# Kernel tuning notes

Hardware: AMD Instinct MI355X
Metric: run time of the kernel (lower is better)

## Reference

```python
import jax, jax.numpy as jnp
import numpy as np

CHAN = 24
INNER = 64
GROUPS = 8
M = 5
LAM = 1e-4
MAX_ITER = 25
BETA = 1.0
EPS = 1e-5
B, HH, WW = 128, 32, 32


def conv2d(x, w, b=None):
    # NCHW, OIHW, 3x3 SAME conv (padding = kernel//2)
    y = jax.lax.conv_general_dilated(x, w, (1, 1), 'SAME',
                                     dimension_numbers=('NCHW', 'OIHW', 'NCHW'))
    if b is not None:
        y = y + b[None, :, None, None]
    return y


def group_norm(x, g, b):
    bsz, c, h, w = x.shape
    xg = x.reshape(bsz, GROUPS, c // GROUPS, h, w)
    mu = xg.mean(axis=(2, 3, 4), keepdims=True)
    var = xg.var(axis=(2, 3, 4), keepdims=True)
    xn = ((xg - mu) / jnp.sqrt(var + EPS)).reshape(bsz, c, h, w)
    return xn * g[None, :, None, None] + b[None, :, None, None]


def batch_norm(x, g, b):
    # training-mode batch statistics over (N, H, W)
    mu = x.mean(axis=(0, 2, 3), keepdims=True)
    var = x.var(axis=(0, 2, 3), keepdims=True)
    return (x - mu) / jnp.sqrt(var + EPS) * g[None, :, None, None] + b[None, :, None, None]


def resnet_f(p, z, x):
    c1w, g1g, g1b, c2w, g2g, g2b, g3g, g3b = p
    y = group_norm(jax.nn.relu(conv2d(z, c1w)), g1g, g1b)
    return group_norm(jax.nn.relu(z + group_norm(x + conv2d(y, c2w), g2g, g2b)), g3g, g3b)


def anderson(f, x0):
    # Anderson acceleration, fixed MAX_ITER iterations (no host-sync tol break).
    bsz = x0.shape[0]
    d = x0.size // bsz
    X = jnp.zeros((bsz, M, d), x0.dtype)
    Fm = jnp.zeros((bsz, M, d), x0.dtype)
    f0 = f(x0).reshape(bsz, -1)
    X = X.at[:, 0].set(x0.reshape(bsz, -1))
    Fm = Fm.at[:, 0].set(f0)
    X = X.at[:, 1].set(f0)
    Fm = Fm.at[:, 1].set(f(f0.reshape(x0.shape)).reshape(bsz, -1))
    for k in range(2, MAX_ITER):
        n = min(k, M)
        G = Fm[:, :n] - X[:, :n]                       # [b, n, d]
        Hm = jnp.zeros((bsz, n + 1, n + 1), x0.dtype)
        Hm = Hm.at[:, 0, 1:].set(1.0).at[:, 1:, 0].set(1.0)
        Hm = Hm.at[:, 1:, 1:].set(jnp.einsum('bnd,bmd->bnm', G, G)
                                  + LAM * jnp.eye(n, dtype=x0.dtype)[None])
        yv = jnp.zeros((bsz, n + 1, 1), x0.dtype).at[:, 0, 0].set(1.0)
        alpha = jnp.linalg.solve(Hm, yv)[:, 1:, 0]     # [b, n]
        xnew = (BETA * jnp.einsum('bn,bnd->bd', alpha, Fm[:, :n])
                + (1.0 - BETA) * jnp.einsum('bn,bnd->bd', alpha, X[:, :n]))
        X = X.at[:, k % M].set(xnew)
        Fm = Fm.at[:, k % M].set(f(xnew.reshape(x0.shape)).reshape(bsz, -1))
    return X[:, (MAX_ITER - 1) % M].reshape(x0.shape)


def setup_inputs() -> dict:
    key = jax.random.key(0)
    ks = jax.random.split(key, 8)
    inp = {
        'x': jax.random.normal(ks[0], (B, 3, HH, WW), jnp.float32),
        'pre_conv_w': jax.random.normal(ks[1], (CHAN, 3, 3, 3), jnp.float32) * 0.1,
        'pre_conv_b': jnp.zeros((CHAN,), jnp.float32),
        'pre_bn_g': jnp.ones((CHAN,), jnp.float32),
        'pre_bn_b': jnp.zeros((CHAN,), jnp.float32),
        'f_conv1_w': jax.random.normal(ks[2], (INNER, CHAN, 3, 3), jnp.float32) * 0.01,
        'gn1_g': jnp.ones((INNER,), jnp.float32),
        'gn1_b': jnp.zeros((INNER,), jnp.float32),
        'f_conv2_w': jax.random.normal(ks[3], (CHAN, INNER, 3, 3), jnp.float32) * 0.01,
        'gn2_g': jnp.ones((CHAN,), jnp.float32),
        'gn2_b': jnp.zeros((CHAN,), jnp.float32),
        'gn3_g': jnp.ones((CHAN,), jnp.float32),
        'gn3_b': jnp.zeros((CHAN,), jnp.float32),
        'post_bn_g': jnp.ones((CHAN,), jnp.float32),
        'post_bn_b': jnp.zeros((CHAN,), jnp.float32),
        'fc_w': jax.random.normal(ks[4], (10, CHAN * 4 * 4), jnp.float32) * 0.05,
        'fc_b': jnp.zeros((10,), jnp.float32),
    }
    return inp


def reference(x, pre_conv_w, pre_conv_b, pre_bn_g, pre_bn_b,
              f_conv1_w, gn1_g, gn1_b, f_conv2_w, gn2_g, gn2_b, gn3_g, gn3_b,
              post_bn_g, post_bn_b, fc_w, fc_b):
    # pre: conv + BatchNorm
    xp = batch_norm(conv2d(x, pre_conv_w, pre_conv_b), pre_bn_g, pre_bn_b)
    p = (f_conv1_w, gn1_g, gn1_b, f_conv2_w, gn2_g, gn2_b, gn3_g, gn3_b)
    # DEQ fixed-point solve (eval path: train=False returns the fixed point)
    z_star = anderson(lambda z: resnet_f(p, z, xp), jnp.zeros_like(xp))
    z = resnet_f(p, z_star, xp)
    # post: relu -> BN -> avgpool(8,8) -> flatten -> linear
    h = batch_norm(jax.nn.relu(z), post_bn_g, post_bn_b)
    bsz, c, hh, ww = h.shape
    pooled = h.reshape(bsz, c, hh // 8, 8, ww // 8, 8).mean(axis=(3, 5))  # [B,C,4,4]
    return pooled.reshape(bsz, -1) @ fc_w.T + fc_b
```

## Files before the change

### kernel.cpp

```cpp
#include <hip/hip_runtime.h>
#include <hip/hip_bf16.h>

typedef __hip_bfloat16 bf16;
typedef unsigned short ushortT;
typedef __attribute__((ext_vector_type(8))) short short8;
typedef __attribute__((ext_vector_type(4))) float f32x4;

#define BB 128
#define CHAN 24
#define INNER 64
#define HW 1024
#define DD (CHAN*HW)

constexpr size_t cBD = (size_t)BB*DD;
constexpr size_t cYB = (size_t)BB*INNER*HW;

__device__ __attribute__((aligned(16))) ushortT g_xp[cBD];
__device__ __attribute__((aligned(16))) ushortT g_X[5*cBD];
__device__ __attribute__((aligned(16))) ushortT g_F[5*cBD];
__device__ __attribute__((aligned(16))) ushortT g_G[5*cBD];
__device__ __attribute__((aligned(16))) ushortT g_yb[cYB];
__device__ __attribute__((aligned(16))) ushortT g_tb[cBD];
__device__ __attribute__((aligned(16))) ushortT g_w1m[9*64*32];
__device__ __attribute__((aligned(16))) ushortT g_w2m[9*24*64];
__device__ __attribute__((aligned(16))) float g_stats2a[48];
__device__ __attribute__((aligned(16))) float g_stats2b[48];
__device__ __attribute__((aligned(16))) float g_gn1sum[BB*8*2];
__device__ __attribute__((aligned(16))) float g_gn2sum[BB*24*2];
__device__ __attribute__((aligned(16))) float g_gram[BB*25];
__device__ __attribute__((aligned(16))) float g_params[5120];
__device__ unsigned g_isbf16;

#define P_PCW 0
#define P_PCB 648
#define P_PBG 672
#define P_PBB 696
#define P_G1G 720
#define P_G1B 784
#define P_G2G 848
#define P_G2B 872
#define P_G3G 896
#define P_G3B 920
#define P_POG 944
#define P_POB 968
#define P_FCW 992
#define P_FCB 4832

__device__ __forceinline__ size_t aidx(int b, int icv, int pix){
  return (((size_t)b*3 + icv)*1024 + (size_t)pix)*8;
}
__device__ __forceinline__ float rdin(const void* p, int i){
  if (g_isbf16) return __bfloat162float(((const bf16*)p)[i]);
  return ((const float*)p)[i];
}
__device__ __forceinline__ float b2f(ushortT u){
  unsigned v = ((unsigned)u) << 16;
  return __builtin_bit_cast(float, v);
}
__device__ __forceinline__ ushortT f2b(float f){
  unsigned u = __builtin_bit_cast(unsigned, f);
  u += 0x7FFFu + ((u >> 16) & 1u);
  return (ushortT)(u >> 16);
}
__device__ __forceinline__ void ld24c(const ushortT* base, int b, int pix, float* o){
  #pragma unroll
  for (int icv=0;icv<3;icv++){
    short8 v = *(const short8*)&base[aidx(b,icv,pix)];
    #pragma unroll
    for (int j=0;j<8;j++) o[icv*8+j] = b2f((ushortT)v[j]);
  }
}
__device__ __forceinline__ void st24c(ushortT* base, int b, int pix, const float* i){
  #pragma unroll
  for (int icv=0;icv<3;icv++){
    short8 v;
    #pragma unroll
    for (int j=0;j<8;j++) v[j] = (short)f2b(i[icv*8+j]);
    *(short8*)&base[aidx(b,icv,pix)] = v;
  }
}

__global__ void detect_k(const void* g1g){
  if (threadIdx.x==0 && blockIdx.x==0){
    unsigned u = *(const unsigned*)g1g;
    g_isbf16 = (u == 0x3F803F80u) ? 1u : 0u;
  }
}

__global__ void cvt_params_k(const void* pcw, const void* pcb, const void* pbg, const void* pbb,
                             const void* g1g, const void* g1b, const void* g2g, const void* g2b,
                             const void* g3g, const void* g3b, const void* pog, const void* pob,
                             const void* fcw, const void* fcb){
  int t = threadIdx.x;
  for (int i=t;i<648;i+=256)  g_params[P_PCW+i]=rdin(pcw,i);
  for (int i=t;i<24;i+=256) { g_params[P_PCB+i]=rdin(pcb,i);
                              g_params[P_PBG+i]=rdin(pbg,i);
                              g_params[P_PBB+i]=rdin(pbb,i);
                              g_params[P_G2G+i]=rdin(g2g,i);
                              g_params[P_G2B+i]=rdin(g2b,i);
                              g_params[P_G3G+i]=rdin(g3g,i);
                              g_params[P_G3B+i]=rdin(g3b,i);
                              g_params[P_POG+i]=rdin(pog,i);
                              g_params[P_POB+i]=rdin(pob,i); }
  for (int i=t;i<64;i+=256) { g_params[P_G1G+i]=rdin(g1g,i);
                              g_params[P_G1B+i]=rdin(g1b,i); }
  for (int i=t;i<3840;i+=256) g_params[P_FCW+i]=rdin(fcw,i);
  for (int i=t;i<10;i+=256)   g_params[P_FCB+i]=rdin(fcb,i);
  for (int i=t;i<48;i+=256) { g_stats2a[i]=0.f; g_stats2b[i]=0.f; }
}

__global__ void wtm_k(const void* w1, const void* w2){
  int t = blockIdx.x*256 + threadIdx.x;
  if (t < 9*64*32){
    int ic = t & 31, oc = (t>>5)&63, s9 = t>>11;
    float v = (ic<24) ? rdin(w1, (oc*24+ic)*9 + s9) : 0.f;
    g_w1m[t] = f2b(v);
  }
  int u = t - 9*64*32;
  if (u >= 0 && u < 9*24*64){
    int ic = u & 63; int rest = u >> 6; int oc = rest % 24; int s9 = rest / 24;
    g_w2m[u] = f2b(rdin(w2, (oc*64+ic)*9 + s9));
  }
}

__global__ void zero0_k(){
  size_t base = ((size_t)blockIdx.x*256 + threadIdx.x)*8;
  short8 z = {0,0,0,0,0,0,0,0};
  *(short8*)&g_yb[base] = z;
  if (blockIdx.x < 1536) *(short8*)&g_X[base] = z;
  int t = blockIdx.x*256 + threadIdx.x;
  if (blockIdx.x < 8)  g_gn1sum[t] = 0.f;
  if (blockIdx.x < 24) g_gn2sum[t] = 0.f;
}

__global__ void preconv_k(const void* __restrict__ x){
  __shared__ float sR2d[4*48];
  int id = blockIdx.x*256 + threadIdx.x;
  int b = id >> 10, pix = id & 1023;
  int yy = pix >> 5, xx = pix & 31;
  float acc[24];
  #pragma unroll
  for (int oc=0;oc<24;oc++) acc[oc] = g_params[P_PCB+oc];
  for (int ic=0; ic<3; ic++)
    for (int ky=0; ky<3; ky++){
      int gy = yy+ky-1; if (gy<0||gy>=32) continue;
      for (int kx=0;kx<3;kx++){
        int gx = xx+kx-1; if (gx<0||gx>=32) continue;
        float v = rdin(x, ((b*3+ic)*32+gy)*32+gx);
        #pragma unroll
        for (int oc=0;oc<24;oc++)
          acc[oc] += v * g_params[P_PCW+(oc*3+ic)*9+ky*3+kx];
      }
    }
  st24c(g_tb, b, pix, acc);
  int lane = threadIdx.x & 63, wv = threadIdx.x >> 6;
  #pragma unroll
  for (int c=0;c<24;c++){
    float r = acc[c], q = acc[c]*acc[c];
    #pragma unroll
    for (int off=32;off;off>>=1){ r += __shfl_down(r,off,64); q += __shfl_down(q,off,64); }
    if (lane==0){ sR2d[wv*48+c*2]=r; sR2d[wv*48+c*2+1]=q; }
  }
  __syncthreads();
  if (threadIdx.x < 48)
    atomicAdd(&g_stats2a[threadIdx.x],
      sR2d[threadIdx.x] + sR2d[48+threadIdx.x] + sR2d[96+threadIdx.x] + sR2d[144+threadIdx.x]);
}

__global__ void bn_apply_k(){
  int id = blockIdx.x*256+threadIdx.x;
  int b = id >> 10, pix = id & 1023;
  const float inv = 1.f/(BB*HW);
  float tv[24], ov[24];
  ld24c(g_tb, b, pix, tv);
  #pragma unroll
  for (int c=0;c<24;c++){
    float mean = g_stats2a[c*2]*inv;
    float var = fmaxf(g_stats2a[c*2+1]*inv - mean*mean, 0.f);
    float rstd = rsqrtf(var + 1e-5f);
    ov[c] = (tv[c]-mean)*rstd*g_params[P_PBG+c] + g_params[P_PBB+c];
  }
  st24c(g_xp, b, pix, ov);
}

__launch_bounds__(256, 2)
__global__ void conv1_k(int s){
  __shared__ ushortT sMem[29312];
  ushortT* sA = sMem;
  ushortT* sW = sMem + 10880;
  const int tid = threadIdx.x;
  const int lane = tid & 63, wv = tid >> 6;
  const int mLane = lane & 15, q = lane >> 4;
  const int b = blockIdx.x >> 2, yt = blockIdx.x & 3;
  const ushortT* __restrict__ Xs = g_X + (size_t)s*cBD;
  if (blockIdx.x < 24) g_gn2sum[blockIdx.x*256 + tid] = 0.f;
  for (int i = tid; i < 1360; i += 256){
    int icv = i & 3, apix = i >> 2;
    int yl = apix / 34, xl = apix - yl*34;
    int gy = yt*8 - 1 + yl, gx = xl - 1;
    short8 v = {0,0,0,0,0,0,0,0};
    if (gy >= 0 && gy < 32 && gx >= 0 && gx < 32 && icv < 3)
      v = *(const short8*)&Xs[aidx(b, icv, gy*32 + gx)];
    *(short8*)&sA[(size_t)(apix*4 + (icv ^ (apix&3)))*8] = v;
  }
  for (int i = tid; i < 2304; i += 256){
    int icv = i & 3, rest = i >> 2;
    int oc = rest & 63, s9 = rest >> 6;
    short8 v = *(const short8*)&g_w1m[(size_t)((s9*64 + oc)*32) + icv*8];
    *(short8*)&sW[(size_t)((s9*64+oc)*4 + (icv ^ (oc&3)))*8] = v;
  }
  __syncthreads();
  f32x4 acc[4][4];
  #pragma unroll
  for (int mt=0;mt<4;mt++)
    #pragma unroll
    for (int nt=0;nt<4;nt++) acc[mt][nt] = (f32x4){0.f,0.f,0.f,0.f};
  for (int s9=0; s9<9; s9++){
    int ky = s9/3, kx = s9 - ky*3;
    short8 bfr[4];
    #pragma unroll
    for (int nt=0;nt<4;nt++){
      int oc = nt*16 + mLane;
      bfr[nt] = *(const short8*)&sW[(size_t)((s9*64+oc)*4 + (q ^ (oc&3)))*8];
    }
    #pragma unroll
    for (int mt=0;mt<4;mt++){
      int g = wv*4+mt;
      int apix = ((g>>1) + ky)*34 + (g&1)*16 + mLane + kx;
      short8 afr = *(const short8*)&sA[(size_t)(apix*4 + (q ^ (apix&3)))*8];
      #pragma unroll
      for (int nt=0;nt<4;nt++)
        acc[mt][nt] = __builtin_amdgcn_mfma_f32_16x16x32_bf16(afr, bfr[nt], acc[mt][nt], 0,0,0);
    }
  }
  __syncthreads();
  ushortT* sOut = sMem;
  #pragma unroll
  for (int mt=0;mt<4;mt++){
    int g = wv*4+mt;
    #pragma unroll
    for (int nt=0;nt<4;nt++){
      int oc = nt*16 + mLane;
      #pragma unroll
      for (int r=0;r<4;r++){
        int pix = (g>>1)*32 + (g&1)*16 + q*4 + r;
        sOut[pix*64 + oc] = f2b(fmaxf(acc[mt][nt][r], 0.f));
      }
    }
  }
  __syncthreads();
  float s0=0.f, s1=0.f;
  size_t gbase = ((size_t)b*1024 + yt*256)*64;
  for (int c = tid; c < 2048; c += 256){
    short8 v = *(const short8*)&sOut[c*8];
    *(short8*)&g_yb[gbase + (size_t)c*8] = v;
    #pragma unroll
    for (int j=0;j<8;j++){ float f = b2f((ushortT)v[j]); s0 += f; s1 += f*f; }
  }
  s0 += __shfl_down(s0,32); s1 += __shfl_down(s1,32);
  s0 += __shfl_down(s0,16); s1 += __shfl_down(s1,16);
  s0 += __shfl_down(s0, 8); s1 += __shfl_down(s1, 8);
  if (lane < 8){
    atomicAdd(&g_gn1sum[(b*8+lane)*2],   s0);
    atomicAdd(&g_gn1sum[(b*8+lane)*2+1], s1);
  }
}

__launch_bounds__(256, 2)
__global__ void conv2_k(){
  __shared__ ushortT sMem[35584];
  __shared__ float sAff[128];
  ushortT* sA = sMem;
  ushortT* sW = sMem + 21760;
  const int tid = threadIdx.x;
  const int lane = tid & 63, wv = tid >> 6;
  const int mLane = lane & 15, q = lane >> 4;
  const int b = blockIdx.x >> 2, yt = blockIdx.x & 3;
  if (tid < 64){
    int c = tid, gr = c>>3;
    float S = g_gn1sum[(b*8+gr)*2], Q = g_gn1sum[(b*8+gr)*2+1];
    float mean = S*(1.f/8192.f);
    float var = fmaxf(Q*(1.f/8192.f) - mean*mean, 0.f);
    float rstd = rsqrtf(var + 1e-5f);
    float sc = rstd*g_params[P_G1G+c];
    sAff[c] = sc; sAff[64+c] = g_params[P_G1B+c] - mean*sc;
  }
  __syncthreads();
  for (int i = tid; i < 2720; i += 256){
    int icv = i & 7, apix = i >> 3;
    int yl = apix / 34, xl = apix - yl*34;
    int gy = yt*8 - 1 + yl, gx = xl - 1;
    short8 v = {0,0,0,0,0,0,0,0};
    if (gy >= 0 && gy < 32 && gx >= 0 && gx < 32){
      short8 raw = *(const short8*)&g_yb[((size_t)b*1024 + gy*32+gx)*64 + icv*8];
      #pragma unroll
      for (int j=0;j<8;j++){
        int c = icv*8+j;
        v[j] = (short)f2b(b2f((ushortT)raw[j])*sAff[c] + sAff[64+c]);
      }
    }
    *(short8*)&sA[(size_t)(apix*8 + (icv ^ (apix&7)))*8] = v;
  }
  for (int i = tid; i < 1728; i += 256){
    int icv = i & 7, rest = i >> 3;
    int oc = rest % 24, s9 = rest / 24;
    short8 v = *(const short8*)&g_w2m[(size_t)((s9*24+oc)*64) + icv*8];
    *(short8*)&sW[(size_t)((s9*24+oc)*8 + (icv ^ (oc&7)))*8] = v;
  }
  __syncthreads();
  f32x4 acc[4][2];
  #pragma unroll
  for (int mt=0;mt<4;mt++){ acc[mt][0]=(f32x4){0.f,0.f,0.f,0.f}; acc[mt][1]=(f32x4){0.f,0.f,0.f,0.f}; }
  const bool nt1ok = (mLane < 8);
  for (int s9=0; s9<9; s9++){
    int ky = s9/3, kx = s9 - ky*3;
    #pragma unroll
    for (int ks=0; ks<2; ks++){
      int ib = ks*4;
      short8 bfr[2];
      { int oc = mLane;
        bfr[0] = *(const short8*)&sW[(size_t)((s9*24+oc)*8 + ((ib+q) ^ (oc&7)))*8]; }
      if (nt1ok){
        int oc = 16 + mLane;
        bfr[1] = *(const short8*)&sW[(size_t)((s9*24+oc)*8 + ((ib+q) ^ (oc&7)))*8];
      } else bfr[1] = (short8){0,0,0,0,0,0,0,0};
      #pragma unroll
      for (int mt=0;mt<4;mt++){
        int g = wv*4+mt;
        int apix = ((g>>1) + ky)*34 + (g&1)*16 + mLane + kx;
        short8 afr = *(const short8*)&sA[(size_t)(apix*8 + ((ib+q) ^ (apix&7)))*8];
        acc[mt][0] = __builtin_amdgcn_mfma_f32_16x16x32_bf16(afr, bfr[0], acc[mt][0], 0,0,0);
        acc[mt][1] = __builtin_amdgcn_mfma_f32_16x16x32_bf16(afr, bfr[1], acc[mt][1], 0,0,0);
      }
    }
  }
  #pragma unroll
  for (int nt=0;nt<2;nt++){
    int oc = nt*16 + mLane;
    bool ok = (oc < 24);
    int icv = oc >> 3, e = oc & 7;
    float s0=0.f, s1=0.f;
    if (ok){
      #pragma unroll
      for (int mt=0;mt<4;mt++){
        int g = wv*4+mt;
        #pragma unroll
        for (int r=0;r<4;r++){
          int pix = (yt*8 + (g>>1))*32 + (g&1)*16 + q*4 + r;
          size_t o = aidx(b, icv, pix) + e;
          float v = acc[mt][nt][r] + b2f(g_xp[o]);
          g_tb[o] = f2b(v);
          s0 += v; s1 += v*v;
        }
      }
    }
    s0 += __shfl_down(s0,32); s1 += __shfl_down(s1,32);
    s0 += __shfl_down(s0,16); s1 += __shfl_down(s1,16);
    if (lane < 16 && ok){
      atomicAdd(&g_gn2sum[(b*24+oc)*2],   s0);
      atomicAdd(&g_gn2sum[(b*24+oc)*2+1], s1);
    }
  }
}

template<int N>
__device__ __forceinline__ void chol_alpha(const float Kf[5][5], float* alpha){
  double K[N][N];
  #pragma unroll
  for (int i=0;i<N;i++)
    #pragma unroll
    for (int j=0;j<N;j++)
      K[i][j] = (double)Kf[i][j] + (i==j ? 1e-4 : 0.0);
  #pragma unroll
  for (int c=0;c<N;c++){
    double d = K[c][c];
    #pragma unroll
    for (int k2=0;k2<c;k2++) d -= K[c][k2]*K[c][k2];
    d = sqrt(fmax(d, 1e-300));
    K[c][c] = d;
    double inv = 1.0/d;
    #pragma unroll
    for (int r=c+1;r<N;r++){
      double v = K[r][c];
      #pragma unroll
      for (int k2=0;k2<c;k2++) v -= K[r][k2]*K[c][k2];
      K[r][c] = v*inv;
    }
  }
  double y[N];
  #pragma unroll
  for (int i=0;i<N;i++){
    double v = 1.0;
    #pragma unroll
    for (int j=0;j<i;j++) v -= K[i][j]*y[j];
    y[i] = v / K[i][i];
  }
  double w[N];
  #pragma unroll
  for (int i=N-1;i>=0;i--){
    double v = y[i];
    #pragma unroll
    for (int j=i+1;j<N;j++) v -= K[j][i]*w[j];
    w[i] = v / K[i][i];
  }
  double sum = 0.0;
  #pragma unroll
  for (int i=0;i<N;i++) sum += w[i];
  double invs = 1.0/sum;
  #pragma unroll
  for (int i=0;i<N;i++) alpha[i] = (float)(w[i]*invs);
}

__launch_bounds__(1024)
__global__ void fuse_k(int s, int n, int snext){
  __shared__ float sM2[8], sR2[8], sM3[8], sR3[8];
  __shared__ float sSc2[24], sSb2[24], sSc3[24], sSb3[24];
  __shared__ float sRed[16*16];
  __shared__ float sRedG[16*5];
  __shared__ float sAlpha[5];
  __shared__ float sStat[16*48];
  const int b = blockIdx.x;
  const int t = threadIdx.x;
  const int lane = t & 63, wv = t >> 6;
  if (t < 16) g_gn1sum[b*16 + t] = 0.f;
  if (t < 8){
    float S = g_gn2sum[(b*24+t*3)*2]   + g_gn2sum[(b*24+t*3+1)*2]   + g_gn2sum[(b*24+t*3+2)*2];
    float Q = g_gn2sum[(b*24+t*3)*2+1] + g_gn2sum[(b*24+t*3+1)*2+1] + g_gn2sum[(b*24+t*3+2)*2+1];
    float m = S*(1.f/3072.f);
    sM2[t] = m;
    sR2[t] = rsqrtf(fmaxf(Q*(1.f/3072.f) - m*m, 0.f) + 1e-5f);
  }
  __syncthreads();
  if (t < 24){
    int g = t/3;
    float sc = sR2[g]*g_params[P_G2G+t];
    sSc2[t] = sc; sSb2[t] = g_params[P_G2B+t] - sM2[g]*sc;
  }
  __syncthreads();
  float xv[24], v[24];
  ld24c(g_tb, b, t, v);
  ld24c(g_X + (size_t)s*cBD, b, t, xv);
  float p0[8], p1[8];
  #pragma unroll
  for (int g=0;g<8;g++){ p0[g]=0.f; p1[g]=0.f; }
  #pragma unroll
  for (int c=0;c<24;c++){
    float val = fmaxf(xv[c] + v[c]*sSc2[c] + sSb2[c], 0.f);
    v[c] = val;
    int g = c/3;
    p0[g] += val; p1[g] += val*val;
  }
  #pragma unroll
  for (int g=0;g<8;g++){
    #pragma unroll
    for (int off=32;off;off>>=1){ p0[g]+=__shfl_down(p0[g],off,64); p1[g]+=__shfl_down(p1[g],off,64); }
  }
  if (lane==0){
    #pragma unroll
    for (int g=0;g<8;g++){ sRed[wv*16+g*2]=p0[g]; sRed[wv*16+g*2+1]=p1[g]; }
  }
  __syncthreads();
  if (t < 8){
    float S=0.f, Q=0.f;
    #pragma unroll
    for (int w=0;w<16;w++){ S += sRed[w*16+t*2]; Q += sRed[w*16+t*2+1]; }
    float m = S*(1.f/3072.f);
    sM3[t] = m;
    sR3[t] = rsqrtf(fmaxf(Q*(1.f/3072.f) - m*m, 0.f) + 1e-5f);
  }
  __syncthreads();
  if (t < 24){
    int g = t/3;
    float sc = sR3[g]*g_params[P_G3G+t];
    sSc3[t] = sc; sSb3[t] = g_params[P_G3B+t] - sM3[g]*sc;
  }
  __syncthreads();
  float fv[24];
  #pragma unroll
  for (int c=0;c<24;c++) fv[c] = v[c]*sSc3[c] + sSb3[c];
  st24c(g_F + (size_t)s*cBD, b, t, fv);

  if (n > 0){
    float gl[24];
    #pragma unroll
    for (int c=0;c<24;c++) gl[c] = b2f(f2b(fv[c] - xv[c]));
    st24c(g_G + (size_t)s*cBD, b, t, gl);
    float part[5];
    #pragma unroll
    for (int j=0;j<5;j++) part[j] = 0.f;
    #pragma unroll
    for (int j=0;j<5;j++){
      if (j >= n) continue;
      float acc = 0.f;
      if (j == s){
        #pragma unroll
        for (int c=0;c<24;c++) acc += gl[c]*gl[c];
      } else {
        float gv[24];
        ld24c(g_G + (size_t)j*cBD, b, t, gv);
        #pragma unroll
        for (int c=0;c<24;c++) acc += gl[c]*gv[c];
      }
      part[j] = acc;
    }
    #pragma unroll
    for (int j=0;j<5;j++){
      float vv = part[j];
      #pragma unroll
      for (int off=32;off;off>>=1) vv += __shfl_down(vv,off,64);
      if (lane==0) sRedG[wv*5+j] = vv;
    }
    __syncthreads();
    if (t == 0){
      for (int j=0;j<n;j++){
        float vv = 0.f;
        for (int w=0;w<16;w++) vv += sRedG[w*5+j];
        g_gram[b*25+s*5+j] = vv;
        g_gram[b*25+j*5+s] = vv;
      }
      float Kf[5][5];
      for (int i=0;i<n;i++)
        for (int j=0;j<n;j++) Kf[i][j] = g_gram[b*25+i*5+j];
      float al[5];
      if (n==1) al[0]=1.f;
      else if (n==2) chol_alpha<2>(Kf, al);
      else if (n==3) chol_alpha<3>(Kf, al);
      else if (n==4) chol_alpha<4>(Kf, al);
      else chol_alpha<5>(Kf, al);
      for (int j=0;j<n;j++) sAlpha[j] = al[j];
    }
    __syncthreads();
    float acc[24];
    #pragma unroll
    for (int c=0;c<24;c++) acc[c] = 0.f;
    #pragma unroll
    for (int j=0;j<5;j++){
      if (j >= n) continue;
      float aj = sAlpha[j];
      if (j == s){
        #pragma unroll
        for (int c=0;c<24;c++) acc[c] += aj*b2f(f2b(fv[c]));
      } else {
        float tv2[24];
        ld24c(g_F + (size_t)j*cBD, b, t, tv2);
        #pragma unroll
        for (int c=0;c<24;c++) acc[c] += aj*tv2[c];
      }
    }
    st24c(g_X + (size_t)snext*cBD, b, t, acc);
  } else {
    #pragma unroll
    for (int c=0;c<24;c++){
      float r = fmaxf(b2f(f2b(fv[c])), 0.f);
      float q = r*r;
      #pragma unroll
      for (int off=32;off;off>>=1){ r += __shfl_down(r,off,64); q += __shfl_down(q,off,64); }
      if (lane==0){ sStat[wv*48+c*2]=r; sStat[wv*48+c*2+1]=q; }
    }
    __syncthreads();
    if (t < 48){
      float vv = 0.f;
      #pragma unroll
      for (int w=0;w<16;w++) vv += sStat[w*48+t];
      atomicAdd(&g_stats2b[t], vv);
    }
  }
}

__global__ void postfc_k(void* __restrict__ out){
  __shared__ float sPool[384];
  __shared__ float sMean[24], sRstd[24];
  int b = blockIdx.x, t = threadIdx.x;
  if (t < 24){
    const float inv = 1.f/(BB*HW);
    float mean = g_stats2b[t*2]*inv;
    float var = fmaxf(g_stats2b[t*2+1]*inv - mean*mean, 0.f);
    sMean[t] = mean; sRstd[t] = rsqrtf(var + 1e-5f);
  }
  __syncthreads();
  const ushortT* z = g_F + 4*cBD;
  for (int i=t; i<384; i+=256){
    int c = i>>4, bin = i&15, ph = bin>>2, pw = bin&3;
    int icv = c>>3, e = c&7;
    float gg = g_params[P_POG+c], bv = g_params[P_POB+c];
    float mean = sMean[c], rstd = sRstd[c];
    float sum = 0.f;
    for (int dy=0;dy<8;dy++)
      for (int dx=0;dx<8;dx++){
        int pix = (ph*8+dy)*32 + pw*8+dx;
        float vv = fmaxf(b2f(z[aidx(b,icv,pix) + e]), 0.f);
        sum += (vv-mean)*rstd*gg + bv;
      }
    sPool[i] = sum*(1.f/64.f);
  }
  __syncthreads();
  if (t < 10){
    float s2 = g_params[P_FCB+t];
    for (int k2=0;k2<384;k2++) s2 += sPool[k2]*g_params[P_FCW+t*384+k2];
    if (g_isbf16) ((bf16*)out)[b*10+t] = __float2bfloat16(s2);
    else ((float*)out)[b*10+t] = s2;
  }
}

extern "C" void kernel_launch(void* const* d_in, const int* in_sizes, int n_in,
                              void* d_out, int out_size, void* d_ws, size_t ws_size,
                              hipStream_t stream){
  const void* x   = d_in[0];
  const void* pcw = d_in[1];
  const void* pcb = d_in[2];
  const void* pbg = d_in[3];
  const void* pbb = d_in[4];
  const void* w1  = d_in[5];
  const void* g1g = d_in[6];
  const void* g1b = d_in[7];
  const void* w2  = d_in[8];
  const void* g2g = d_in[9];
  const void* g2b = d_in[10];
  const void* g3g = d_in[11];
  const void* g3b = d_in[12];
  const void* pog = d_in[13];
  const void* pob = d_in[14];
  const void* fcw = d_in[15];
  const void* fcb = d_in[16];
  (void)d_ws; (void)ws_size; (void)in_sizes; (void)n_in; (void)out_size;

  detect_k<<<1,64,0,stream>>>(g1g);
  cvt_params_k<<<1,256,0,stream>>>(pcw,pcb,pbg,pbb,g1g,g1b,g2g,g2b,g3g,g3b,pog,pob,fcw,fcb);
  wtm_k<<<126,256,0,stream>>>(w1, w2);

  preconv_k<<<512,256,0,stream>>>(x);
  bn_apply_k<<<512,256,0,stream>>>();

  zero0_k<<<4096,256,0,stream>>>();
  conv2_k<<<512,256,0,stream>>>();
  fuse_k<<<128,1024,0,stream>>>(0, 1, 1);

  for (int k=1;k<25;k++){
    int s = k%5;
    conv1_k<<<512,256,0,stream>>>(s);
    conv2_k<<<512,256,0,stream>>>();
    if (k < 24){
      int n = (k+1 < 5) ? (k+1) : 5;
      fuse_k<<<128,1024,0,stream>>>(s, n, (k+1)%5);
    } else {
      fuse_k<<<128,1024,0,stream>>>(s, 0, -1);
    }
  }

  postfc_k<<<128,256,0,stream>>>(d_out);
}
```

Measured before the change: 1.452 ms.

## Fuse conv2 into per-sample Anderson fuse kernel using whole-image shared memory

Merges the second convolution (conv2_k) into the fuse kernel. One 1024-thread block per sample now stages the whole normalized 64-channel image plus the weights in about 160KB of dynamic shared memory. GroupNorm-2 statistics are reduced in shared memory instead of through global atomics, and the intermediate g_tb no longer round-trips through global memory. This removes a launch and global traffic on every iteration. The cost is only 128 blocks of 1024 threads with one block per CU, so parallelism and occupancy for the MFMA conv are lower than the previous 512-block conv2 launch.

```diff
diff --git a/kernel.cpp b/kernel.cpp
--- a/kernel.cpp
+++ b/kernel.cpp
@@ -26,7 +26,6 @@
 __device__ __attribute__((aligned(16))) float g_stats2a[48];
 __device__ __attribute__((aligned(16))) float g_stats2b[48];
 __device__ __attribute__((aligned(16))) float g_gn1sum[BB*8*2];
-__device__ __attribute__((aligned(16))) float g_gn2sum[BB*24*2];
 __device__ __attribute__((aligned(16))) float g_gram[BB*25];
 __device__ __attribute__((aligned(16))) float g_params[5120];
 __device__ unsigned g_isbf16;
@@ -130,7 +129,6 @@
   if (blockIdx.x < 1536) *(short8*)&g_X[base] = z;
   int t = blockIdx.x*256 + threadIdx.x;
   if (blockIdx.x < 8)  g_gn1sum[t] = 0.f;
-  if (blockIdx.x < 24) g_gn2sum[t] = 0.f;
 }
 
 __global__ void preconv_k(const void* __restrict__ x){
@@ -193,7 +191,6 @@
   const int mLane = lane & 15, q = lane >> 4;
   const int b = blockIdx.x >> 2, yt = blockIdx.x & 3;
   const ushortT* __restrict__ Xs = g_X + (size_t)s*cBD;
-  if (blockIdx.x < 24) g_gn2sum[blockIdx.x*256 + tid] = 0.f;
   for (int i = tid; i < 1360; i += 256){
     int icv = i & 3, apix = i >> 2;
     int yl = apix / 34, xl = apix - yl*34;
@@ -266,103 +263,6 @@
   }
 }
 
-__launch_bounds__(256, 2)
-__global__ void conv2_k(){
-  __shared__ ushortT sMem[35584];
-  __shared__ float sAff[128];
-  ushortT* sA = sMem;
-  ushortT* sW = sMem + 21760;
-  const int tid = threadIdx.x;
-  const int lane = tid & 63, wv = tid >> 6;
-  const int mLane = lane & 15, q = lane >> 4;
-  const int b = blockIdx.x >> 2, yt = blockIdx.x & 3;
-  if (tid < 64){
-    int c = tid, gr = c>>3;
-    float S = g_gn1sum[(b*8+gr)*2], Q = g_gn1sum[(b*8+gr)*2+1];
-    float mean = S*(1.f/8192.f);
-    float var = fmaxf(Q*(1.f/8192.f) - mean*mean, 0.f);
-    float rstd = rsqrtf(var + 1e-5f);
-    float sc = rstd*g_params[P_G1G+c];
-    sAff[c] = sc; sAff[64+c] = g_params[P_G1B+c] - mean*sc;
-  }
-  __syncthreads();
-  for (int i = tid; i < 2720; i += 256){
-    int icv = i & 7, apix = i >> 3;
-    int yl = apix / 34, xl = apix - yl*34;
-    int gy = yt*8 - 1 + yl, gx = xl - 1;
-    short8 v = {0,0,0,0,0,0,0,0};
-    if (gy >= 0 && gy < 32 && gx >= 0 && gx < 32){
-      short8 raw = *(const short8*)&g_yb[((size_t)b*1024 + gy*32+gx)*64 + icv*8];
-      #pragma unroll
-      for (int j=0;j<8;j++){
-        int c = icv*8+j;
-        v[j] = (short)f2b(b2f((ushortT)raw[j])*sAff[c] + sAff[64+c]);
-      }
-    }
-    *(short8*)&sA[(size_t)(apix*8 + (icv ^ (apix&7)))*8] = v;
-  }
-  for (int i = tid; i < 1728; i += 256){
-    int icv = i & 7, rest = i >> 3;
-    int oc = rest % 24, s9 = rest / 24;
-    short8 v = *(const short8*)&g_w2m[(size_t)((s9*24+oc)*64) + icv*8];
-    *(short8*)&sW[(size_t)((s9*24+oc)*8 + (icv ^ (oc&7)))*8] = v;
-  }
-  __syncthreads();
-  f32x4 acc[4][2];
-  #pragma unroll
-  for (int mt=0;mt<4;mt++){ acc[mt][0]=(f32x4){0.f,0.f,0.f,0.f}; acc[mt][1]=(f32x4){0.f,0.f,0.f,0.f}; }
-  const bool nt1ok = (mLane < 8);
-  for (int s9=0; s9<9; s9++){
-    int ky = s9/3, kx = s9 - ky*3;
-    #pragma unroll
-    for (int ks=0; ks<2; ks++){
-      int ib = ks*4;
-      short8 bfr[2];
-      { int oc = mLane;
-        bfr[0] = *(const short8*)&sW[(size_t)((s9*24+oc)*8 + ((ib+q) ^ (oc&7)))*8]; }
-      if (nt1ok){
-        int oc = 16 + mLane;
-        bfr[1] = *(const short8*)&sW[(size_t)((s9*24+oc)*8 + ((ib+q) ^ (oc&7)))*8];
-      } else bfr[1] = (short8){0,0,0,0,0,0,0,0};
-      #pragma unroll
-      for (int mt=0;mt<4;mt++){
-        int g = wv*4+mt;
-        int apix = ((g>>1) + ky)*34 + (g&1)*16 + mLane + kx;
-        short8 afr = *(const short8*)&sA[(size_t)(apix*8 + ((ib+q) ^ (apix&7)))*8];
-        acc[mt][0] = __builtin_amdgcn_mfma_f32_16x16x32_bf16(afr, bfr[0], acc[mt][0], 0,0,0);
-        acc[mt][1] = __builtin_amdgcn_mfma_f32_16x16x32_bf16(afr, bfr[1], acc[mt][1], 0,0,0);
-      }
-    }
-  }
-  #pragma unroll
-  for (int nt=0;nt<2;nt++){
-    int oc = nt*16 + mLane;
-    bool ok = (oc < 24);
-    int icv = oc >> 3, e = oc & 7;
-    float s0=0.f, s1=0.f;
-    if (ok){
-      #pragma unroll
-      for (int mt=0;mt<4;mt++){
-        int g = wv*4+mt;
-        #pragma unroll
-        for (int r=0;r<4;r++){
-          int pix = (yt*8 + (g>>1))*32 + (g&1)*16 + q*4 + r;
-          size_t o = aidx(b, icv, pix) + e;
-          float v = acc[mt][nt][r] + b2f(g_xp[o]);
-          g_tb[o] = f2b(v);
-          s0 += v; s1 += v*v;
-        }
-      }
-    }
-    s0 += __shfl_down(s0,32); s1 += __shfl_down(s1,32);
-    s0 += __shfl_down(s0,16); s1 += __shfl_down(s1,16);
-    if (lane < 16 && ok){
-      atomicAdd(&g_gn2sum[(b*24+oc)*2],   s0);
-      atomicAdd(&g_gn2sum[(b*24+oc)*2+1], s1);
-    }
-  }
-}
-
 template<int N>
 __device__ __forceinline__ void chol_alpha(const float Kf[5][5], float* alpha){
   double K[N][N];
@@ -411,41 +311,157 @@
   for (int i=0;i<N;i++) alpha[i] = (float)(w[i]*invs);
 }
 
+#define C2F_SMEM 161440
+
 __launch_bounds__(1024)
-__global__ void fuse_k(int s, int n, int snext){
-  __shared__ float sM2[8], sR2[8], sM3[8], sR3[8];
-  __shared__ float sSc2[24], sSb2[24], sSc3[24], sSb3[24];
-  __shared__ float sRed[16*16];
-  __shared__ float sRedG[16*5];
-  __shared__ float sAlpha[5];
-  __shared__ float sStat[16*48];
+__global__ void c2f_k(int s, int n, int snext){
+  extern __shared__ __align__(16) ushortT sU[];
+  ushortT* sYb = sU;
+  ushortT* sTB = sU;
+  ushortT* sW2 = sU + 65536;
+  float* sS    = (float*)(sU + 79360);
+  float* sAff1  = sS;
+  float* sStat2 = sS + 128;
+  float* sAff2  = sS + 176;
+  float* sStat3 = sS + 224;
+  float* sAff3  = sS + 240;
+  float* sRed   = sS + 288;
+  float* sRedG  = sS + 544;
+  float* sAlpha = sS + 624;
+  float* sFin   = (float*)sTB;
+
   const int b = blockIdx.x;
   const int t = threadIdx.x;
   const int lane = t & 63, wv = t >> 6;
+  const int mLane = lane & 15, q = lane >> 4;
+  const int g0 = wv*4;
+  const bool ntOK = (mLane < 8);
+  const bool fin = (n == 0);
+
+  if (t < 64){
+    const int c = t, gr = c>>3;
+    float S = g_gn1sum[(b*8+gr)*2], Q = g_gn1sum[(b*8+gr)*2+1];
+    float mean = S*(1.f/8192.f);
+    float var  = fmaxf(Q*(1.f/8192.f) - mean*mean, 0.f);
+    float rstd = rsqrtf(var + 1e-5f);
+    float sc = rstd*g_params[P_G1G+c];
+    sAff1[c] = sc; sAff1[64+c] = g_params[P_G1B+c] - mean*sc;
+  }
   if (t < 16) g_gn1sum[b*16 + t] = 0.f;
-  if (t < 8){
-    float S = g_gn2sum[(b*24+t*3)*2]   + g_gn2sum[(b*24+t*3+1)*2]   + g_gn2sum[(b*24+t*3+2)*2];
-    float Q = g_gn2sum[(b*24+t*3)*2+1] + g_gn2sum[(b*24+t*3+1)*2+1] + g_gn2sum[(b*24+t*3+2)*2+1];
+  if (t >= 64 && t < 112) sStat2[t-64] = 0.f;
+  if (t >= 112 && t < 128) sStat3[t-112] = 0.f;
+  __syncthreads();
+
+  for (int i=t; i<8192; i+=1024){
+    int chk = i & 7, pix = i >> 3;
+    short8 raw = *(const short8*)&g_yb[((size_t)b*1024 + pix)*64 + chk*8];
+    short8 v;
+    #pragma unroll
+    for (int j=0;j<8;j++){
+      int c = chk*8+j;
+      v[j] = (short)f2b(b2f((ushortT)raw[j])*sAff1[c] + sAff1[64+c]);
+    }
+    *(short8*)&sYb[(size_t)(pix*8 + (chk^(pix&7)))*8] = v;
+  }
+  for (int i=t; i<1728; i+=1024){
+    int icv=i&7, rest=i>>3, oc=rest%24, s9=rest/24;
+    *(short8*)&sW2[(size_t)((s9*24+oc)*8 + (icv^(oc&7)))*8] =
+      *(const short8*)&g_w2m[(size_t)((s9*24+oc)*64) + icv*8];
+  }
+  __syncthreads();
+
+  f32x4 a2[4][2];
+  #pragma unroll
+  for (int mt=0;mt<4;mt++){ a2[mt][0]=(f32x4){0.f,0.f,0.f,0.f}; a2[mt][1]=(f32x4){0.f,0.f,0.f,0.f}; }
+  for (int s9=0; s9<9; ++s9){
+    const int ky = s9/3, kx = s9 - ky*3;
+    #pragma unroll
+    for (int ks=0; ks<2; ++ks){
+      const int ch = ks*4 + q;
+      short8 b0 = *(const short8*)&sW2[(size_t)((s9*24+mLane)*8 + (ch^(mLane&7)))*8];
+      short8 b1 = ntOK ? *(const short8*)&sW2[(size_t)((s9*24+16+mLane)*8 + (ch^(mLane&7)))*8]
+                       : (short8){0,0,0,0,0,0,0,0};
+      #pragma unroll
+      for (int mt=0;mt<4;mt++){
+        const int g = g0+mt;
+        const int gy = (g>>1) + ky - 1;
+        const int gx = (g&1)*16 + mLane + kx - 1;
+        short8 afr = {0,0,0,0,0,0,0,0};
+        if (gy>=0 && gy<32 && gx>=0 && gx<32){
+          const int pp = gy*32 + gx;
+          afr = *(const short8*)&sYb[(size_t)(pp*8 + (ch^(pp&7)))*8];
+        }
+        a2[mt][0] = __builtin_amdgcn_mfma_f32_16x16x32_bf16(afr, b0, a2[mt][0], 0,0,0);
+        a2[mt][1] = __builtin_amdgcn_mfma_f32_16x16x32_bf16(afr, b1, a2[mt][1], 0,0,0);
+      }
+    }
+  }
+  #pragma unroll
+  for (int ci=0; ci<2; ++ci){
+    const int oc = ci*16 + mLane;
+    const bool ok = (ci==0) || ntOK;
+    const int icv = oc>>3, e = oc&7;
+    float s0=0.f, s1=0.f;
+    if (ok){
+      #pragma unroll
+      for (int mt=0;mt<4;mt++){
+        #pragma unroll
+        for (int r=0;r<4;r++){
+          const int pp = (g0+mt)*16 + q*4 + r;
+          float v = a2[mt][ci][r] + b2f(g_xp[aidx(b,icv,pp)+e]);
+          a2[mt][ci][r] = v;
+          s0 += v; s1 += v*v;
+        }
+      }
+    }
+    s0 += __shfl_down(s0,32); s1 += __shfl_down(s1,32);
+    s0 += __shfl_down(s0,16); s1 += __shfl_down(s1,16);
+    if (lane < 16 && ok){
+      atomicAdd(&sStat2[oc*2],   s0);
+      atomicAdd(&sStat2[oc*2+1], s1);
+    }
+  }
+  __syncthreads();
+
+  #pragma unroll
+  for (int ci=0; ci<2; ++ci){
+    const int oc = ci*16 + mLane;
+    if ((ci==0) || ntOK){
+      const int icv = oc>>3, e = oc&7;
+      #pragma unroll
+      for (int mt=0;mt<4;mt++)
+        #pragma unroll
+        for (int r=0;r<4;r++){
+          const int pp = (g0+mt)*16 + q*4 + r;
+          sTB[(size_t)(pp*4 + (icv ^ ((pp>>2)&3)))*8 + e] = f2b(a2[mt][ci][r]);
+        }
+    }
+  }
+  if (t < 24){
+    const int gr = t/3;
+    float S = sStat2[(gr*3)*2]  +sStat2[(gr*3+1)*2]  +sStat2[(gr*3+2)*2];
+    float Q = sStat2[(gr*3)*2+1]+sStat2[(gr*3+1)*2+1]+sStat2[(gr*3+2)*2+1];
     float m = S*(1.f/3072.f);
-    sM2[t] = m;
-    sR2[t] = rsqrtf(fmaxf(Q*(1.f/3072.f) - m*m, 0.f) + 1e-5f);
-  }
-  __syncthreads();
-  if (t < 24){
-    int g = t/3;
-    float sc = sR2[g]*g_params[P_G2G+t];
-    sSc2[t] = sc; sSb2[t] = g_params[P_G2B+t] - sM2[g]*sc;
-  }
-  __syncthreads();
-  float xv[24], v[24];
-  ld24c(g_tb, b, t, v);
+    float rstd = rsqrtf(fmaxf(Q*(1.f/3072.f)-m*m,0.f)+1e-5f);
+    float sc = rstd*g_params[P_G2G+t];
+    sAff2[t] = sc; sAff2[24+t] = g_params[P_G2B+t] - m*sc;
+  }
+  __syncthreads();
+
+  float v[24], xv[24];
+  #pragma unroll
+  for (int i=0;i<3;i++){
+    short8 t8 = *(const short8*)&sTB[(size_t)(t*4 + (i ^ ((t>>2)&3)))*8];
+    #pragma unroll
+    for (int j8=0;j8<8;j8++) v[i*8+j8] = b2f((ushortT)t8[j8]);
+  }
   ld24c(g_X + (size_t)s*cBD, b, t, xv);
   float p0[8], p1[8];
   #pragma unroll
   for (int g=0;g<8;g++){ p0[g]=0.f; p1[g]=0.f; }
   #pragma unroll
   for (int c=0;c<24;c++){
-    float val = fmaxf(xv[c] + v[c]*sSc2[c] + sSb2[c], 0.f);
+    float val = fmaxf(xv[c] + v[c]*sAff2[c] + sAff2[24+c], 0.f);
     v[c] = val;
     int g = c/3;
     p0[g] += val; p1[g] += val*val;
@@ -465,43 +481,44 @@
     #pragma unroll
     for (int w=0;w<16;w++){ S += sRed[w*16+t*2]; Q += sRed[w*16+t*2+1]; }
     float m = S*(1.f/3072.f);
-    sM3[t] = m;
-    sR3[t] = rsqrtf(fmaxf(Q*(1.f/3072.f) - m*m, 0.f) + 1e-5f);
+    sStat3[t*2]   = m;
+    sStat3[t*2+1] = rsqrtf(fmaxf(Q*(1.f/3072.f) - m*m, 0.f) + 1e-5f);
   }
   __syncthreads();
   if (t < 24){
     int g = t/3;
-    float sc = sR3[g]*g_params[P_G3G+t];
-    sSc3[t] = sc; sSb3[t] = g_params[P_G3B+t] - sM3[g]*sc;
+    float sc = sStat3[g*2+1]*g_params[P_G3G+t];
+    sAff3[t] = sc; sAff3[24+t] = g_params[P_G3B+t] - sStat3[g*2]*sc;
   }
   __syncthreads();
   float fv[24];
   #pragma unroll
-  for (int c=0;c<24;c++) fv[c] = v[c]*sSc3[c] + sSb3[c];
+  for (int c=0;c<24;c++) fv[c] = v[c]*sAff3[c] + sAff3[24+c];
   st24c(g_F + (size_t)s*cBD, b, t, fv);
 
-  if (n > 0){
+  if (!fin){
     float gl[24];
     #pragma unroll
     for (int c=0;c<24;c++) gl[c] = b2f(f2b(fv[c] - xv[c]));
     st24c(g_G + (size_t)s*cBD, b, t, gl);
     float part[5];
     #pragma unroll
-    for (int j=0;j<5;j++) part[j] = 0.f;
+    for (int j=0;j<5;j++) part[j]=0.f;
     #pragma unroll
     for (int j=0;j<5;j++){
-      if (j >= n) continue;
-      float acc = 0.f;
-      if (j == s){
-        #pragma unroll
-        for (int c=0;c<24;c++) acc += gl[c]*gl[c];
-      } else {
-        float gv[24];
-        ld24c(g_G + (size_t)j*cBD, b, t, gv);
-        #pragma unroll
-        for (int c=0;c<24;c++) acc += gl[c]*gv[c];
-      }
-      part[j] = acc;
+      if (j < n){
+        float acc=0.f;
+        if (j == s){
+          #pragma unroll
+          for (int c=0;c<24;c++) acc += gl[c]*gl[c];
+        } else {
+          float gv[24];
+          ld24c(g_G + (size_t)j*cBD, b, t, gv);
+          #pragma unroll
+          for (int c=0;c<24;c++) acc += gl[c]*gv[c];
+        }
+        part[j] = acc;
+      }
     }
     #pragma unroll
     for (int j=0;j<5;j++){
@@ -530,38 +547,41 @@
       for (int j=0;j<n;j++) sAlpha[j] = al[j];
     }
     __syncthreads();
-    float acc[24];
-    #pragma unroll
-    for (int c=0;c<24;c++) acc[c] = 0.f;
+    float al[5];
+    #pragma unroll
+    for (int j=0;j<5;j++) al[j] = (j<n) ? sAlpha[j] : 0.f;
+    float xn[24];
+    #pragma unroll
+    for (int c=0;c<24;c++) xn[c] = 0.f;
     #pragma unroll
     for (int j=0;j<5;j++){
-      if (j >= n) continue;
-      float aj = sAlpha[j];
-      if (j == s){
-        #pragma unroll
-        for (int c=0;c<24;c++) acc[c] += aj*b2f(f2b(fv[c]));
-      } else {
-        float tv2[24];
-        ld24c(g_F + (size_t)j*cBD, b, t, tv2);
-        #pragma unroll
-        for (int c=0;c<24;c++) acc[c] += aj*tv2[c];
-      }
-    }
-    st24c(g_X + (size_t)snext*cBD, b, t, acc);
+      if (j < n){
+        if (j == s){
+          #pragma unroll
+          for (int c=0;c<24;c++) xn[c] += al[j]*b2f(f2b(fv[c]));
+        } else {
+          float fv2[24];
+          ld24c(g_F + (size_t)j*cBD, b, t, fv2);
+          #pragma unroll
+          for (int c=0;c<24;c++) xn[c] += al[j]*fv2[c];
+        }
+      }
+    }
+    st24c(g_X + (size_t)snext*cBD, b, t, xn);
   } else {
     #pragma unroll
     for (int c=0;c<24;c++){
       float r = fmaxf(b2f(f2b(fv[c])), 0.f);
-      float q = r*r;
-      #pragma unroll
-      for (int off=32;off;off>>=1){ r += __shfl_down(r,off,64); q += __shfl_down(q,off,64); }
-      if (lane==0){ sStat[wv*48+c*2]=r; sStat[wv*48+c*2+1]=q; }
+      float q2 = r*r;
+      #pragma unroll
+      for (int off=32;off;off>>=1){ r += __shfl_down(r,off,64); q2 += __shfl_down(q2,off,64); }
+      if (lane==0){ sFin[wv*48+c*2]=r; sFin[wv*48+c*2+1]=q2; }
     }
     __syncthreads();
     if (t < 48){
       float vv = 0.f;
       #pragma unroll
-      for (int w=0;w<16;w++) vv += sStat[w*48+t];
+      for (int w=0;w<16;w++) vv += sFin[w*48+t];
       atomicAdd(&g_stats2b[t], vv);
     }
   }
@@ -624,6 +644,13 @@
   const void* fcb = d_in[16];
   (void)d_ws; (void)ws_size; (void)in_sizes; (void)n_in; (void)out_size;
 
+  static bool attrSet = false;
+  if (!attrSet){
+    hipFuncSetAttribute(reinterpret_cast<const void*>(c2f_k),
+                        hipFuncAttributeMaxDynamicSharedMemorySize, C2F_SMEM);
+    attrSet = true;
+  }
+
   detect_k<<<1,64,0,stream>>>(g1g);
   cvt_params_k<<<1,256,0,stream>>>(pcw,pcb,pbg,pbb,g1g,g1b,g2g,g2b,g3g,g3b,pog,pob,fcw,fcb);
   wtm_k<<<126,256,0,stream>>>(w1, w2);
@@ -632,18 +659,16 @@
   bn_apply_k<<<512,256,0,stream>>>();
 
   zero0_k<<<4096,256,0,stream>>>();
-  conv2_k<<<512,256,0,stream>>>();
-  fuse_k<<<128,1024,0,stream>>>(0, 1, 1);
+  c2f_k<<<128,1024,C2F_SMEM,stream>>>(0, 1, 1);
 
   for (int k=1;k<25;k++){
     int s = k%5;
     conv1_k<<<512,256,0,stream>>>(s);
-    conv2_k<<<512,256,0,stream>>>();
     if (k < 24){
       int n = (k+1 < 5) ? (k+1) : 5;
-      fuse_k<<<128,1024,0,stream>>>(s, n, (k+1)%5);
+      c2f_k<<<128,1024,C2F_SMEM,stream>>>(s, n, (k+1)%5);
     } else {
-      fuse_k<<<128,1024,0,stream>>>(s, 0, -1);
+      c2f_k<<<128,1024,C2F_SMEM,stream>>>(s, 0, 0);
     }
   }
 
```

Measured after the change: 1.382 ms. -4.8%, faster.
